# Kernel tuning notes

Hardware: AMD Instinct MI355X
Metric: run time of the kernel (lower is better)

Reference implementation:

```python
import jax, jax.numpy as jnp
import numpy as np

RATE = 2          # attention_rate from __init__
SOFTMAX_SCALE = 10.0  # standard contextual-attention temperature
EPS = 1e-8


def setup_inputs() -> dict:
    key = jax.random.key(0)
    k1, k2 = jax.random.split(key)
    x = jax.random.normal(k1, (1, 128, 192, 192), dtype=jnp.float32)
    # binary hole mask: 1 = hole (to be filled), 0 = valid background
    mask = (jax.random.uniform(k2, (1, 1, 192, 192)) < 0.25).astype(jnp.float32)
    return {"x": x, "mask": mask}


def reference(x, mask):
    b, c, h, w = x.shape
    r = RATE
    hs, ws = h // r, w // r
    n = hs * ws

    # F.interpolate(..., mode='nearest') downsample == strided slice when divisible
    xs = x[:, :, ::r, ::r]            # [b, c, hs, ws]
    ms = mask[:, :, ::r, ::r]         # [b, 1, hs, ws]

    feat = xs.reshape(b, c, n)        # queries (raw) and keys (normalized)
    keys = feat / (jnp.sqrt(jnp.sum(feat * feat, axis=1, keepdims=True)) + EPS)

    # conv-based correlation == all-pairs inner product with normalized bg patches
    scores = jnp.einsum('bcn,bcm->bnm', feat, keys) * SOFTMAX_SCALE  # [b, n, n]

    valid = (ms.reshape(b, 1, n) == 0.0)  # background key locations
    scores = jnp.where(valid, scores, -1e4)
    attn = jax.nn.softmax(scores, axis=-1)
    attn = attn * valid                   # zero out hole keys exactly

    # extract non-overlapping r x r patches from full-res x: [b, n, c*r*r]
    patches = (x.reshape(b, c, hs, r, ws, r)
                 .transpose(0, 2, 4, 1, 3, 5)
                 .reshape(b, n, c * r * r))

    # transposed-conv reconstruction == weighted sum of patches, folded back
    recon = jnp.einsum('bnm,bmd->bnd', attn, patches)   # [b, n, c*r*r]
    recon_img = (recon.reshape(b, hs, ws, c, r, r)
                      .transpose(0, 3, 1, 4, 2, 5)
                      .reshape(b, c, h, w))

    # composite: keep known pixels, fill holes with attended reconstruction
    return x * (1.0 - mask) + recon_img * mask
```

## Files before the change

### kernel.cpp

```cpp
#include <hip/hip_runtime.h>
#include <hip/hip_bf16.h>

typedef _Float16 f16x8 __attribute__((ext_vector_type(8)));
typedef _Float16 f16x4 __attribute__((ext_vector_type(4)));
typedef float    f32x4 __attribute__((ext_vector_type(4)));

#define HW   36864
#define W_   192
#define NS   9216
#define CCH  128
#define DV   512
#define ROWS 64
#define KV   64
#define NT   144

__global__ __launch_bounds__(256) void prep_vt_kernel(const float* __restrict__ x,
        _Float16* __restrict__ Vt, _Float16* __restrict__ F16)
{
    int m = blockIdx.x * 256 + threadIdx.x;
    int d = blockIdx.y;
    int c = d >> 2, di = (d >> 1) & 1, dj = d & 1;
    int i = m / 96, j = m - i * 96;
    float v = x[c * HW + (2 * i + di) * W_ + (2 * j + dj)];
    _Float16 h = (_Float16)v;
    Vt[(size_t)d * NS + m] = h;
    if ((d & 3) == 0) F16[m * CCH + c] = h;
}

__global__ __launch_bounds__(64) void prep_csv_kernel(const _Float16* __restrict__ F16,
        const float* __restrict__ mask, float* __restrict__ csv)
{
    int m = blockIdx.x;
    int t = threadIdx.x;
    float a = (float)F16[m * CCH + 2 * t];
    float b = (float)F16[m * CCH + 2 * t + 1];
    float ss = a * a + b * b;
    #pragma unroll
    for (int off = 1; off <= 32; off <<= 1)
        ss += __shfl_xor(ss, off);
    if (t == 0) {
        int i = m / 96, j = m - i * 96;
        float ms = mask[(2 * i) * W_ + 2 * j];
        csv[m] = (ms == 0.0f) ? 10.0f / (sqrtf(ss) + 1e-8f) : 0.0f;
    }
}

template<int KT>
__global__ __launch_bounds__(256, 3) void flash_kernel(const _Float16* __restrict__ F16,
        const _Float16* __restrict__ Vt, const float* __restrict__ csv,
        _Float16* __restrict__ po, float* __restrict__ av)
{
    constexpr int SPLT = NT / KT;
    __shared__ __align__(16) _Float16 Kb[2][KV * CCH];
    __shared__ __align__(16) _Float16 Pb[2][ROWS * KV];
    __shared__ __align__(16) float    abuf[2][ROWS];
    __shared__ __align__(16) int      flags[2][4];
    __shared__ __align__(16) float    lbuf[ROWS];

    const int tid  = threadIdx.x;
    const int wv   = tid >> 6;
    const int lane = tid & 63;
    const int g    = lane >> 4, c16 = lane & 15;
    const int flat = blockIdx.x;
    const int sp   = flat % SPLT;
    const int rest = flat / SPLT;
    const int n0   = (rest >> 1) * ROWS;
    const int d0   = (rest & 1) * 256;
    const int t0   = sp * KT;
    const int sw   = c16 & 7;

    auto stageK = [&](int nb, int t) {
        #pragma unroll
        for (int j = 0; j < 4; ++j) {
            const int key  = wv * 16 + j * 4 + g;
            const int csrc = (c16 & 8) | ((c16 & 7) ^ (key & 7));
            __builtin_amdgcn_global_load_lds(
                (const __attribute__((address_space(1))) void*)
                    (F16 + (size_t)(t * KV + key) * CCH + csrc * 8),
                (__attribute__((address_space(3))) void*)
                    (&Kb[nb][(wv * 16 + j * 4) * CCH]),
                16, 0, 0);
        }
    };

    f16x8 q[4];
    #pragma unroll
    for (int kk = 0; kk < 4; ++kk)
        q[kk] = *(const f16x8*)(F16 + (n0 + wv * 16 + c16) * CCH + kk * 32 + g * 8);

    f32x4 o[4][4];
    #pragma unroll
    for (int rf = 0; rf < 4; ++rf)
        #pragma unroll
        for (int df = 0; df < 4; ++df) o[rf][df] = 0.0f;
    float m_run = -1e30f, l_run = 0.0f;

    const _Float16* vbase = Vt + (size_t)(d0 + wv * 64 + c16) * NS + g * 8;

    stageK(0, t0);
    __syncthreads();

    for (int tl = 0; tl < KT; ++tl) {
        const int buf = tl & 1;
        const int m0  = (t0 + tl) * KV;

        f16x8 vreg[8];
        #pragma unroll
        for (int kf = 0; kf < 2; ++kf)
            #pragma unroll
            for (int df = 0; df < 4; ++df)
                vreg[kf * 4 + df] = *(const f16x8*)(vbase + (size_t)(df * 16) * NS
                                                    + m0 + kf * 32);

        f32x4 s[4];
        #pragma unroll
        for (int cf = 0; cf < 4; ++cf) s[cf] = 0.0f;
        #pragma unroll
        for (int cf = 0; cf < 4; ++cf) {
            const _Float16* kr = &Kb[buf][(cf * 16 + c16) * CCH];
            #pragma unroll
            for (int kk = 0; kk < 4; ++kk) {
                const int c  = kk * 4 + g;
                const int cc = (c & 8) | ((c & 7) ^ sw);
                s[cf] = __builtin_amdgcn_mfma_f32_16x16x32_f16(
                            *(const f16x8*)(kr + cc * 8), q[kk], s[cf], 0, 0, 0);
            }
        }

        f32x4 cs[4];
        #pragma unroll
        for (int cf = 0; cf < 4; ++cf)
            cs[cf] = *(const f32x4*)(csv + m0 + cf * 16 + g * 4);

        float tm = -1e30f;
        #pragma unroll
        for (int cf = 0; cf < 4; ++cf)
            #pragma unroll
            for (int r = 0; r < 4; ++r)
                tm = fmaxf(tm, (cs[cf][r] > 0.0f) ? s[cf][r] * cs[cf][r] : -1e30f);
        tm = fmaxf(tm, __shfl_xor(tm, 16));
        tm = fmaxf(tm, __shfl_xor(tm, 32));

        float al = 1.0f;
        const bool trig = __any(tm > m_run + 8.0f);
        if (trig) {
            float nm = fmaxf(m_run, tm);
            al = __expf(m_run - nm);
            l_run *= al; m_run = nm;
        }
        if (lane == 0) flags[buf][wv] = trig ? 1 : 0;
        if (g == 0)    abuf[buf][wv * 16 + c16] = al;

        float ps = 0.0f;
        const int prow = wv * 16 + c16;
        #pragma unroll
        for (int cf = 0; cf < 4; ++cf) {
            f16x4 ph;
            #pragma unroll
            for (int r = 0; r < 4; ++r) {
                float e = (cs[cf][r] > 0.0f) ? __expf(s[cf][r] * cs[cf][r] - m_run) : 0.0f;
                ps += e;
                ph[r] = (_Float16)e;
            }
            const int ch = (cf * 2 + (g >> 1)) ^ sw;
            *(f16x4*)(&Pb[buf][prow * KV + ch * 8 + (g & 1) * 4]) = ph;
        }
        ps += __shfl_xor(ps, 16);
        ps += __shfl_xor(ps, 32);
        l_run += ps;

        if (tl + 1 < KT) stageK(buf ^ 1, t0 + tl + 1);

        __syncthreads();

        {
            const int4 fl = *(const int4*)(&flags[buf][0]);
            if (fl.x | fl.y | fl.z | fl.w) {
                #pragma unroll
                for (int rf = 0; rf < 4; ++rf) {
                    f32x4 a4 = *(const f32x4*)(&abuf[buf][rf * 16 + g * 4]);
                    #pragma unroll
                    for (int df = 0; df < 4; ++df)
                        #pragma unroll
                        for (int r = 0; r < 4; ++r) o[rf][df][r] *= a4[r];
                }
            }
        }
        #pragma unroll
        for (int kf = 0; kf < 2; ++kf) {
            f16x8 pa[4];
            #pragma unroll
            for (int rf = 0; rf < 4; ++rf)
                pa[rf] = *(const f16x8*)(&Pb[buf][(rf * 16 + c16) * KV
                                                  + (((kf * 4 + g) ^ sw) * 8)]);
            #pragma unroll
            for (int df = 0; df < 4; ++df)
                #pragma unroll
                for (int rf = 0; rf < 4; ++rf)
                    o[rf][df] = __builtin_amdgcn_mfma_f32_16x16x32_f16(
                                    pa[rf], vreg[kf * 4 + df], o[rf][df], 0, 0, 0);
        }
    }

    if (g == 0) {
        lbuf[wv * 16 + c16] = (l_run > 0.0f) ? 1.0f / l_run : 0.0f;
        if (d0 == 0)
            av[sp * NS + n0 + wv * 16 + c16] =
                (l_run > 0.0f) ? m_run + __logf(l_run) : -1e30f;
    }
    __syncthreads();
    #pragma unroll
    for (int rf = 0; rf < 4; ++rf) {
        f32x4 li = *(const f32x4*)(&lbuf[rf * 16 + g * 4]);
        #pragma unroll
        for (int df = 0; df < 4; ++df) {
            f16x4 res;
            #pragma unroll
            for (int r = 0; r < 4; ++r) res[r] = (_Float16)(o[rf][df][r] * li[r]);
            *(f16x4*)(po + ((size_t)sp * DV + d0 + wv * 64 + df * 16 + c16) * NS
                          + n0 + rf * 16 + g * 4) = res;
        }
    }
}

template<int S>
__global__ __launch_bounds__(192) void combine_kernel(const float* __restrict__ x,
        const float* __restrict__ mask, const _Float16* __restrict__ po,
        const float* __restrict__ av, float* __restrict__ out)
{
    int i = blockIdx.x;
    int c = blockIdx.y;
    int w = threadIdx.x;
    int n = i * 96 + (w >> 1);

    float A = -1e30f;
    #pragma unroll
    for (int s = 0; s < S; ++s) A = fmaxf(A, av[s * NS + n]);
    float wt[S], wsum = 0.0f;
    #pragma unroll
    for (int s = 0; s < S; ++s) {
        float a = av[s * NS + n];
        float e = (a > -1e29f) ? __expf(a - A) : 0.0f;
        wt[s] = e; wsum += e;
    }
    float invw = (wsum > 0.0f) ? 1.0f / wsum : 0.0f;

    #pragma unroll
    for (int di = 0; di < 2; ++di) {
        int h = 2 * i + di;
        int d = c * 4 + di * 2 + (w & 1);
        float rv = 0.0f;
        #pragma unroll
        for (int s = 0; s < S; ++s)
            rv += wt[s] * (float)po[((size_t)s * DV + d) * NS + n];
        rv *= invw;
        float xv = x[c * HW + h * W_ + w];
        float mv = mask[h * W_ + w];
        out[c * HW + h * W_ + w] = xv * (1.0f - mv) + rv * mv;
    }
}

extern "C" void kernel_launch(void* const* d_in, const int* in_sizes, int n_in,
                              void* d_out, int out_size, void* d_ws, size_t ws_size,
                              hipStream_t stream) {
    const float* x    = (const float*)d_in[0];
    const float* mask = (const float*)d_in[1];
    float* out = (float*)d_out;

    char* ws = (char*)d_ws;
    _Float16* Vt  = (_Float16*)(ws);
    _Float16* F16 = (_Float16*)(ws + 9437184);
    float*    csv = (float*)   (ws + 11796480);
    float*    av  = (float*)   (ws + 11833344);
    _Float16* po  = (_Float16*)(ws + 12128256);

    prep_vt_kernel <<<dim3(36, 512), 256, 0, stream>>>(x, Vt, F16);
    prep_csv_kernel<<<NS, 64, 0, stream>>>(F16, mask, csv);

    const size_t base = 12128256ull;
    if (ws_size >= base + 8ull * 9437184ull) {
        flash_kernel<18><<<288 * 8, 256, 0, stream>>>(F16, Vt, csv, po, av);
        combine_kernel<8><<<dim3(96, 128), 192, 0, stream>>>(x, mask, po, av, out);
    } else {
        flash_kernel<36><<<288 * 4, 256, 0, stream>>>(F16, Vt, csv, po, av);
        combine_kernel<4><<<dim3(96, 128), 192, 0, stream>>>(x, mask, po, av, out);
    }
}
```

Measured before the change: 341.7 us.

## Use exp2 softmax with additive mask bias, earlier K prefetch, MFMA priority

Folds log2(e) into the per-key scale and adds a precomputed additive bias (-60000 for hole keys), so the inner loop becomes an FMA plus exp2 with no select. The K tile prefetch is issued at the top of each iteration so it overlaps the QK MFMAs. Global address offsets are precomputed, and s_setprio raises wave priority around the MFMA blocks. It adds a second small per-key array read each tile and changes the log-sum-exp output to base-2 scaling. The initial running max becomes a finite sentinel, which risks wrong handling when every key in a split is masked.

```diff
diff --git a/kernel.cpp b/kernel.cpp
--- a/kernel.cpp
+++ b/kernel.cpp
@@ -13,6 +13,11 @@
 #define ROWS 64
 #define KV   64
 #define NT   144
+#define LOG2E 1.44269504089f
+#define LN2   0.69314718056f
+#define THR2  11.5417f
+
+#define EXP2(x) __builtin_exp2f(x)
 
 __global__ __launch_bounds__(256) void prep_vt_kernel(const float* __restrict__ x,
         _Float16* __restrict__ Vt, _Float16* __restrict__ F16)
@@ -28,7 +33,7 @@
 }
 
 __global__ __launch_bounds__(64) void prep_csv_kernel(const _Float16* __restrict__ F16,
-        const float* __restrict__ mask, float* __restrict__ csv)
+        const float* __restrict__ mask, float* __restrict__ csv, float* __restrict__ csb)
 {
     int m = blockIdx.x;
     int t = threadIdx.x;
@@ -41,14 +46,16 @@
     if (t == 0) {
         int i = m / 96, j = m - i * 96;
         float ms = mask[(2 * i) * W_ + 2 * j];
-        csv[m] = (ms == 0.0f) ? 10.0f / (sqrtf(ss) + 1e-8f) : 0.0f;
+        bool valid = (ms == 0.0f);
+        csv[m] = valid ? 10.0f * LOG2E / (sqrtf(ss) + 1e-8f) : 0.0f;
+        csb[m] = valid ? 0.0f : -60000.0f;
     }
 }
 
 template<int KT>
 __global__ __launch_bounds__(256, 3) void flash_kernel(const _Float16* __restrict__ F16,
         const _Float16* __restrict__ Vt, const float* __restrict__ csv,
-        _Float16* __restrict__ po, float* __restrict__ av)
+        const float* __restrict__ csb, _Float16* __restrict__ po, float* __restrict__ av)
 {
     constexpr int SPLT = NT / KT;
     __shared__ __align__(16) _Float16 Kb[2][KV * CCH];
@@ -69,19 +76,30 @@
     const int t0   = sp * KT;
     const int sw   = c16 & 7;
 
+    int koff[4];
+    #pragma unroll
+    for (int j = 0; j < 4; ++j) {
+        const int key  = wv * 16 + j * 4 + g;
+        const int csrc = (c16 & 8) | ((c16 & 7) ^ (key & 7));
+        koff[j] = (key * CCH + csrc * 8) * 2;
+    }
     auto stageK = [&](int nb, int t) {
-        #pragma unroll
-        for (int j = 0; j < 4; ++j) {
-            const int key  = wv * 16 + j * 4 + g;
-            const int csrc = (c16 & 8) | ((c16 & 7) ^ (key & 7));
+        const char* src = (const char*)F16 + (size_t)t * (KV * CCH * 2);
+        #pragma unroll
+        for (int j = 0; j < 4; ++j)
             __builtin_amdgcn_global_load_lds(
-                (const __attribute__((address_space(1))) void*)
-                    (F16 + (size_t)(t * KV + key) * CCH + csrc * 8),
-                (__attribute__((address_space(3))) void*)
-                    (&Kb[nb][(wv * 16 + j * 4) * CCH]),
+                (const __attribute__((address_space(1))) void*)(src + koff[j]),
+                (__attribute__((address_space(3))) void*)(&Kb[nb][(wv * 16 + j * 4) * CCH]),
                 16, 0, 0);
-        }
     };
+
+    int voff[8];
+    #pragma unroll
+    for (int kf = 0; kf < 2; ++kf)
+        #pragma unroll
+        for (int df = 0; df < 4; ++df)
+            voff[kf * 4 + df] = (int)(((size_t)(d0 + wv * 64 + df * 16 + c16) * NS
+                                       + kf * 32 + g * 8) * 2);
 
     f16x8 q[4];
     #pragma unroll
@@ -93,9 +111,7 @@
     for (int rf = 0; rf < 4; ++rf)
         #pragma unroll
         for (int df = 0; df < 4; ++df) o[rf][df] = 0.0f;
-    float m_run = -1e30f, l_run = 0.0f;
-
-    const _Float16* vbase = Vt + (size_t)(d0 + wv * 64 + c16) * NS + g * 8;
+    float m_run = -20000.0f, l_run = 0.0f;
 
     stageK(0, t0);
     __syncthreads();
@@ -104,17 +120,18 @@
         const int buf = tl & 1;
         const int m0  = (t0 + tl) * KV;
 
+        if (tl + 1 < KT) stageK(buf ^ 1, t0 + tl + 1);
+
+        const char* vt = (const char*)Vt + (size_t)m0 * 2;
         f16x8 vreg[8];
         #pragma unroll
-        for (int kf = 0; kf < 2; ++kf)
-            #pragma unroll
-            for (int df = 0; df < 4; ++df)
-                vreg[kf * 4 + df] = *(const f16x8*)(vbase + (size_t)(df * 16) * NS
-                                                    + m0 + kf * 32);
+        for (int i = 0; i < 8; ++i)
+            vreg[i] = *(const f16x8*)(vt + voff[i]);
 
         f32x4 s[4];
         #pragma unroll
         for (int cf = 0; cf < 4; ++cf) s[cf] = 0.0f;
+        __builtin_amdgcn_s_setprio(1);
         #pragma unroll
         for (int cf = 0; cf < 4; ++cf) {
             const _Float16* kr = &Kb[buf][(cf * 16 + c16) * CCH];
@@ -126,26 +143,33 @@
                             *(const f16x8*)(kr + cc * 8), q[kk], s[cf], 0, 0, 0);
             }
         }
-
-        f32x4 cs[4];
+        __builtin_amdgcn_s_setprio(0);
+
+        const float* csvt = csv + m0;
+        const float* csbt = csb + m0;
+        f32x4 cs[4], cb[4];
+        #pragma unroll
+        for (int cf = 0; cf < 4; ++cf) {
+            cs[cf] = *(const f32x4*)(csvt + cf * 16 + g * 4);
+            cb[cf] = *(const f32x4*)(csbt + cf * 16 + g * 4);
+        }
+
+        float tm = -1e30f;
         #pragma unroll
         for (int cf = 0; cf < 4; ++cf)
-            cs[cf] = *(const f32x4*)(csv + m0 + cf * 16 + g * 4);
-
-        float tm = -1e30f;
-        #pragma unroll
-        for (int cf = 0; cf < 4; ++cf)
-            #pragma unroll
-            for (int r = 0; r < 4; ++r)
-                tm = fmaxf(tm, (cs[cf][r] > 0.0f) ? s[cf][r] * cs[cf][r] : -1e30f);
+            #pragma unroll
+            for (int r = 0; r < 4; ++r) {
+                s[cf][r] = __builtin_fmaf(s[cf][r], cs[cf][r], cb[cf][r]);
+                tm = fmaxf(tm, s[cf][r]);
+            }
         tm = fmaxf(tm, __shfl_xor(tm, 16));
         tm = fmaxf(tm, __shfl_xor(tm, 32));
 
         float al = 1.0f;
-        const bool trig = __any(tm > m_run + 8.0f);
+        const bool trig = __any(tm > m_run + THR2);
         if (trig) {
             float nm = fmaxf(m_run, tm);
-            al = __expf(m_run - nm);
+            al = EXP2(m_run - nm);
             l_run *= al; m_run = nm;
         }
         if (lane == 0) flags[buf][wv] = trig ? 1 : 0;
@@ -155,21 +179,18 @@
         const int prow = wv * 16 + c16;
         #pragma unroll
         for (int cf = 0; cf < 4; ++cf) {
-            f16x4 ph;
-            #pragma unroll
-            for (int r = 0; r < 4; ++r) {
-                float e = (cs[cf][r] > 0.0f) ? __expf(s[cf][r] * cs[cf][r] - m_run) : 0.0f;
-                ps += e;
-                ph[r] = (_Float16)e;
-            }
+            float e0 = EXP2(s[cf][0] - m_run);
+            float e1 = EXP2(s[cf][1] - m_run);
+            float e2 = EXP2(s[cf][2] - m_run);
+            float e3 = EXP2(s[cf][3] - m_run);
+            ps += (e0 + e1) + (e2 + e3);
+            f16x4 ph = { (_Float16)e0, (_Float16)e1, (_Float16)e2, (_Float16)e3 };
             const int ch = (cf * 2 + (g >> 1)) ^ sw;
             *(f16x4*)(&Pb[buf][prow * KV + ch * 8 + (g & 1) * 4]) = ph;
         }
         ps += __shfl_xor(ps, 16);
         ps += __shfl_xor(ps, 32);
         l_run += ps;
-
-        if (tl + 1 < KT) stageK(buf ^ 1, t0 + tl + 1);
 
         __syncthreads();
 
@@ -186,6 +207,7 @@
                 }
             }
         }
+        __builtin_amdgcn_s_setprio(1);
         #pragma unroll
         for (int kf = 0; kf < 2; ++kf) {
             f16x8 pa[4];
@@ -200,13 +222,14 @@
                     o[rf][df] = __builtin_amdgcn_mfma_f32_16x16x32_f16(
                                     pa[rf], vreg[kf * 4 + df], o[rf][df], 0, 0, 0);
         }
+        __builtin_amdgcn_s_setprio(0);
     }
 
     if (g == 0) {
         lbuf[wv * 16 + c16] = (l_run > 0.0f) ? 1.0f / l_run : 0.0f;
         if (d0 == 0)
             av[sp * NS + n0 + wv * 16 + c16] =
-                (l_run > 0.0f) ? m_run + __logf(l_run) : -1e30f;
+                (l_run > 0.0f) ? m_run * LN2 + __logf(l_run) : -1e30f;
     }
     __syncthreads();
     #pragma unroll
@@ -271,18 +294,19 @@
     _Float16* Vt  = (_Float16*)(ws);
     _Float16* F16 = (_Float16*)(ws + 9437184);
     float*    csv = (float*)   (ws + 11796480);
-    float*    av  = (float*)   (ws + 11833344);
-    _Float16* po  = (_Float16*)(ws + 12128256);
+    float*    csb = (float*)   (ws + 11833344);
+    float*    av  = (float*)   (ws + 11870208);
+    _Float16* po  = (_Float16*)(ws + 12165120);
 
     prep_vt_kernel <<<dim3(36, 512), 256, 0, stream>>>(x, Vt, F16);
-    prep_csv_kernel<<<NS, 64, 0, stream>>>(F16, mask, csv);
-
-    const size_t base = 12128256ull;
+    prep_csv_kernel<<<NS, 64, 0, stream>>>(F16, mask, csv, csb);
+
+    const size_t base = 12165120ull;
     if (ws_size >= base + 8ull * 9437184ull) {
-        flash_kernel<18><<<288 * 8, 256, 0, stream>>>(F16, Vt, csv, po, av);
+        flash_kernel<18><<<288 * 8, 256, 0, stream>>>(F16, Vt, csv, csb, po, av);
         combine_kernel<8><<<dim3(96, 128), 192, 0, stream>>>(x, mask, po, av, out);
     } else {
-        flash_kernel<36><<<288 * 4, 256, 0, stream>>>(F16, Vt, csv, po, av);
+        flash_kernel<36><<<288 * 4, 256, 0, stream>>>(F16, Vt, csv, csb, po, av);
         combine_kernel<4><<<dim3(96, 128), 192, 0, stream>>>(x, mask, po, av, out);
     }
 }
```

New measurement: 528.3 us. 1.55x slower.

## Halve key tile to 32, use exp2 with prescaled scores, raise occupancy, add setprio

Applied to the files above, without the earlier changes.

Cuts the flash kernel's key tile from 64 to 32 keys and doubles the tile count per split, so the K/P shared buffers and the score and V registers shrink. Launch bounds are raised to 4 waves per SIMD to fit more blocks per CU. The softmax moves to base-2 by folding log2(e) into the per-key scale, so exp2 is used directly, masking is applied once, and the rescale threshold and final logsumexp are adjusted to match. s_setprio is added around the MFMA sections, and the P swizzle changes to suit the narrower tile. Smaller tiles mean twice as many loop iterations and barriers per block, with less MFMA work to hide them.

```diff
diff --git a/kernel.cpp b/kernel.cpp
--- a/kernel.cpp
+++ b/kernel.cpp
@@ -11,8 +11,12 @@
 #define CCH  128
 #define DV   512
 #define ROWS 64
-#define KV   64
-#define NT   144
+#define KV   32
+#define NT2  288
+#define LOG2E 1.44269504089f
+#define LN2   0.69314718056f
+#define THR2  11.5417f
+#define EXP2(x) __builtin_exp2f(x)
 
 __global__ __launch_bounds__(256) void prep_vt_kernel(const float* __restrict__ x,
         _Float16* __restrict__ Vt, _Float16* __restrict__ F16)
@@ -41,16 +45,16 @@
     if (t == 0) {
         int i = m / 96, j = m - i * 96;
         float ms = mask[(2 * i) * W_ + 2 * j];
-        csv[m] = (ms == 0.0f) ? 10.0f / (sqrtf(ss) + 1e-8f) : 0.0f;
+        csv[m] = (ms == 0.0f) ? 10.0f * LOG2E / (sqrtf(ss) + 1e-8f) : 0.0f;
     }
 }
 
 template<int KT>
-__global__ __launch_bounds__(256, 3) void flash_kernel(const _Float16* __restrict__ F16,
+__global__ __launch_bounds__(256, 4) void flash_kernel(const _Float16* __restrict__ F16,
         const _Float16* __restrict__ Vt, const float* __restrict__ csv,
         _Float16* __restrict__ po, float* __restrict__ av)
 {
-    constexpr int SPLT = NT / KT;
+    constexpr int SPLT = NT2 / KT;
     __shared__ __align__(16) _Float16 Kb[2][KV * CCH];
     __shared__ __align__(16) _Float16 Pb[2][ROWS * KV];
     __shared__ __align__(16) float    abuf[2][ROWS];
@@ -71,14 +75,14 @@
 
     auto stageK = [&](int nb, int t) {
         #pragma unroll
-        for (int j = 0; j < 4; ++j) {
-            const int key  = wv * 16 + j * 4 + g;
+        for (int j = 0; j < 2; ++j) {
+            const int key  = wv * 8 + j * 4 + g;
             const int csrc = (c16 & 8) | ((c16 & 7) ^ (key & 7));
             __builtin_amdgcn_global_load_lds(
                 (const __attribute__((address_space(1))) void*)
                     (F16 + (size_t)(t * KV + key) * CCH + csrc * 8),
                 (__attribute__((address_space(3))) void*)
-                    (&Kb[nb][(wv * 16 + j * 4) * CCH]),
+                    (&Kb[nb][(wv * 8 + j * 4) * CCH]),
                 16, 0, 0);
         }
     };
@@ -93,7 +97,7 @@
     for (int rf = 0; rf < 4; ++rf)
         #pragma unroll
         for (int df = 0; df < 4; ++df) o[rf][df] = 0.0f;
-    float m_run = -1e30f, l_run = 0.0f;
+    float m_run = -20000.0f, l_run = 0.0f;
 
     const _Float16* vbase = Vt + (size_t)(d0 + wv * 64 + c16) * NS + g * 8;
 
@@ -104,19 +108,16 @@
         const int buf = tl & 1;
         const int m0  = (t0 + tl) * KV;
 
-        f16x8 vreg[8];
-        #pragma unroll
-        for (int kf = 0; kf < 2; ++kf)
-            #pragma unroll
-            for (int df = 0; df < 4; ++df)
-                vreg[kf * 4 + df] = *(const f16x8*)(vbase + (size_t)(df * 16) * NS
-                                                    + m0 + kf * 32);
-
-        f32x4 s[4];
-        #pragma unroll
-        for (int cf = 0; cf < 4; ++cf) s[cf] = 0.0f;
-        #pragma unroll
-        for (int cf = 0; cf < 4; ++cf) {
+        f16x8 vreg[4];
+        #pragma unroll
+        for (int df = 0; df < 4; ++df)
+            vreg[df] = *(const f16x8*)(vbase + (size_t)(df * 16) * NS + m0);
+
+        f32x4 s[2];
+        s[0] = 0.0f; s[1] = 0.0f;
+        __builtin_amdgcn_s_setprio(1);
+        #pragma unroll
+        for (int cf = 0; cf < 2; ++cf) {
             const _Float16* kr = &Kb[buf][(cf * 16 + c16) * CCH];
             #pragma unroll
             for (int kk = 0; kk < 4; ++kk) {
@@ -126,26 +127,29 @@
                             *(const f16x8*)(kr + cc * 8), q[kk], s[cf], 0, 0, 0);
             }
         }
-
-        f32x4 cs[4];
-        #pragma unroll
-        for (int cf = 0; cf < 4; ++cf)
-            cs[cf] = *(const f32x4*)(csv + m0 + cf * 16 + g * 4);
+        __builtin_amdgcn_s_setprio(0);
+
+        f32x4 cs[2];
+        cs[0] = *(const f32x4*)(csv + m0 + g * 4);
+        cs[1] = *(const f32x4*)(csv + m0 + 16 + g * 4);
 
         float tm = -1e30f;
         #pragma unroll
-        for (int cf = 0; cf < 4; ++cf)
-            #pragma unroll
-            for (int r = 0; r < 4; ++r)
-                tm = fmaxf(tm, (cs[cf][r] > 0.0f) ? s[cf][r] * cs[cf][r] : -1e30f);
+        for (int cf = 0; cf < 2; ++cf)
+            #pragma unroll
+            for (int r = 0; r < 4; ++r) {
+                float v = (cs[cf][r] > 0.0f) ? s[cf][r] * cs[cf][r] : -60000.0f;
+                s[cf][r] = v;
+                tm = fmaxf(tm, v);
+            }
         tm = fmaxf(tm, __shfl_xor(tm, 16));
         tm = fmaxf(tm, __shfl_xor(tm, 32));
 
         float al = 1.0f;
-        const bool trig = __any(tm > m_run + 8.0f);
+        const bool trig = __any(tm > m_run + THR2);
         if (trig) {
             float nm = fmaxf(m_run, tm);
-            al = __expf(m_run - nm);
+            al = EXP2(m_run - nm);
             l_run *= al; m_run = nm;
         }
         if (lane == 0) flags[buf][wv] = trig ? 1 : 0;
@@ -154,15 +158,14 @@
         float ps = 0.0f;
         const int prow = wv * 16 + c16;
         #pragma unroll
-        for (int cf = 0; cf < 4; ++cf) {
-            f16x4 ph;
-            #pragma unroll
-            for (int r = 0; r < 4; ++r) {
-                float e = (cs[cf][r] > 0.0f) ? __expf(s[cf][r] * cs[cf][r] - m_run) : 0.0f;
-                ps += e;
-                ph[r] = (_Float16)e;
-            }
-            const int ch = (cf * 2 + (g >> 1)) ^ sw;
+        for (int cf = 0; cf < 2; ++cf) {
+            float e0 = EXP2(s[cf][0] - m_run);
+            float e1 = EXP2(s[cf][1] - m_run);
+            float e2 = EXP2(s[cf][2] - m_run);
+            float e3 = EXP2(s[cf][3] - m_run);
+            ps += (e0 + e1) + (e2 + e3);
+            f16x4 ph = { (_Float16)e0, (_Float16)e1, (_Float16)e2, (_Float16)e3 };
+            const int ch = (cf * 2 + (g >> 1)) ^ (c16 & 3);
             *(f16x4*)(&Pb[buf][prow * KV + ch * 8 + (g & 1) * 4]) = ph;
         }
         ps += __shfl_xor(ps, 16);
@@ -186,27 +189,28 @@
                 }
             }
         }
-        #pragma unroll
-        for (int kf = 0; kf < 2; ++kf) {
+        __builtin_amdgcn_s_setprio(1);
+        {
             f16x8 pa[4];
             #pragma unroll
             for (int rf = 0; rf < 4; ++rf)
                 pa[rf] = *(const f16x8*)(&Pb[buf][(rf * 16 + c16) * KV
-                                                  + (((kf * 4 + g) ^ sw) * 8)]);
+                                                  + ((g ^ (c16 & 3)) * 8)]);
             #pragma unroll
             for (int df = 0; df < 4; ++df)
                 #pragma unroll
                 for (int rf = 0; rf < 4; ++rf)
                     o[rf][df] = __builtin_amdgcn_mfma_f32_16x16x32_f16(
-                                    pa[rf], vreg[kf * 4 + df], o[rf][df], 0, 0, 0);
-        }
+                                    pa[rf], vreg[df], o[rf][df], 0, 0, 0);
+        }
+        __builtin_amdgcn_s_setprio(0);
     }
 
     if (g == 0) {
         lbuf[wv * 16 + c16] = (l_run > 0.0f) ? 1.0f / l_run : 0.0f;
         if (d0 == 0)
             av[sp * NS + n0 + wv * 16 + c16] =
-                (l_run > 0.0f) ? m_run + __logf(l_run) : -1e30f;
+                (l_run > 0.0f) ? m_run * LN2 + __logf(l_run) : -1e30f;
     }
     __syncthreads();
     #pragma unroll
@@ -279,10 +283,10 @@
 
     const size_t base = 12128256ull;
     if (ws_size >= base + 8ull * 9437184ull) {
-        flash_kernel<18><<<288 * 8, 256, 0, stream>>>(F16, Vt, csv, po, av);
+        flash_kernel<36><<<288 * 8, 256, 0, stream>>>(F16, Vt, csv, po, av);
         combine_kernel<8><<<dim3(96, 128), 192, 0, stream>>>(x, mask, po, av, out);
     } else {
-        flash_kernel<36><<<288 * 4, 256, 0, stream>>>(F16, Vt, csv, po, av);
+        flash_kernel<72><<<288 * 4, 256, 0, stream>>>(F16, Vt, csv, po, av);
         combine_kernel<4><<<dim3(96, 128), 192, 0, stream>>>(x, mask, po, av, out);
     }
 }
```

Measured after the change: 462.9 us. 1.35x slower.

## Software-pipeline QK and PV MFMAs across tiles with base-2 softmax

Applied to the files above, without the earlier changes.

Restructures the flash-attention loop so the PV matmul for the previous tile is interleaved with the QK matmul of the current tile. This lets the matrix units overlap with the softmax of the next step, and V loads are issued after the MFMAs to hide their latency. The softmax moves to exp2 by folding log2(e) into the key scale, and masked keys now go through a large negative constant instead of a branch. s_setprio hints are added around the MFMA blocks. In exchange there are more live registers (vreg carried across iterations) and occupancy may suffer.

```diff
diff --git a/kernel.cpp b/kernel.cpp
--- a/kernel.cpp
+++ b/kernel.cpp
@@ -13,6 +13,10 @@
 #define ROWS 64
 #define KV   64
 #define NT   144
+#define LOG2E 1.44269504089f
+#define LN2   0.69314718056f
+#define THR2  11.5417f
+#define EXP2(x) __builtin_exp2f(x)
 
 __global__ __launch_bounds__(256) void prep_vt_kernel(const float* __restrict__ x,
         _Float16* __restrict__ Vt, _Float16* __restrict__ F16)
@@ -41,7 +45,7 @@
     if (t == 0) {
         int i = m / 96, j = m - i * 96;
         float ms = mask[(2 * i) * W_ + 2 * j];
-        csv[m] = (ms == 0.0f) ? 10.0f / (sqrtf(ss) + 1e-8f) : 0.0f;
+        csv[m] = (ms == 0.0f) ? 10.0f * LOG2E / (sqrtf(ss) + 1e-8f) : 0.0f;
     }
 }
 
@@ -93,31 +97,83 @@
     for (int rf = 0; rf < 4; ++rf)
         #pragma unroll
         for (int df = 0; df < 4; ++df) o[rf][df] = 0.0f;
-    float m_run = -1e30f, l_run = 0.0f;
+    float m_run = -20000.0f, l_run = 0.0f;
 
     const _Float16* vbase = Vt + (size_t)(d0 + wv * 64 + c16) * NS + g * 8;
+    f16x8 vreg[8];
 
     stageK(0, t0);
     __syncthreads();
 
-    for (int tl = 0; tl < KT; ++tl) {
-        const int buf = tl & 1;
-        const int m0  = (t0 + tl) * KV;
-
-        f16x8 vreg[8];
-        #pragma unroll
-        for (int kf = 0; kf < 2; ++kf)
-            #pragma unroll
-            for (int df = 0; df < 4; ++df)
-                vreg[kf * 4 + df] = *(const f16x8*)(vbase + (size_t)(df * 16) * NS
-                                                    + m0 + kf * 32);
-
+    auto softmax_store = [&](int kb, int m0, f32x4* s) {
+        f32x4 cs[4];
+        #pragma unroll
+        for (int cf = 0; cf < 4; ++cf)
+            cs[cf] = *(const f32x4*)(csv + m0 + cf * 16 + g * 4);
+        float tm = -1e30f;
+        #pragma unroll
+        for (int cf = 0; cf < 4; ++cf)
+            #pragma unroll
+            for (int r = 0; r < 4; ++r) {
+                float v = (cs[cf][r] > 0.0f) ? s[cf][r] * cs[cf][r] : -60000.0f;
+                s[cf][r] = v;
+                tm = fmaxf(tm, v);
+            }
+        tm = fmaxf(tm, __shfl_xor(tm, 16));
+        tm = fmaxf(tm, __shfl_xor(tm, 32));
+        float al = 1.0f;
+        const bool trig = __any(tm > m_run + THR2);
+        if (trig) {
+            float nm = fmaxf(m_run, tm);
+            al = EXP2(m_run - nm);
+            l_run *= al; m_run = nm;
+        }
+        if (lane == 0) flags[kb][wv] = trig ? 1 : 0;
+        if (g == 0)    abuf[kb][wv * 16 + c16] = al;
+        float ps = 0.0f;
+        const int prow = wv * 16 + c16;
+        #pragma unroll
+        for (int cf = 0; cf < 4; ++cf) {
+            float e0 = EXP2(s[cf][0] - m_run);
+            float e1 = EXP2(s[cf][1] - m_run);
+            float e2 = EXP2(s[cf][2] - m_run);
+            float e3 = EXP2(s[cf][3] - m_run);
+            ps += (e0 + e1) + (e2 + e3);
+            f16x4 ph = { (_Float16)e0, (_Float16)e1, (_Float16)e2, (_Float16)e3 };
+            const int ch = (cf * 2 + (g >> 1)) ^ sw;
+            *(f16x4*)(&Pb[kb][prow * KV + ch * 8 + (g & 1) * 4]) = ph;
+        }
+        ps += __shfl_xor(ps, 16);
+        ps += __shfl_xor(ps, 32);
+        l_run += ps;
+    };
+
+    auto rescale = [&](int pb) {
+        const int4 fl = *(const int4*)(&flags[pb][0]);
+        if (fl.x | fl.y | fl.z | fl.w) {
+            #pragma unroll
+            for (int rf = 0; rf < 4; ++rf) {
+                f32x4 a4 = *(const f32x4*)(&abuf[pb][rf * 16 + g * 4]);
+                #pragma unroll
+                for (int df = 0; df < 4; ++df)
+                    #pragma unroll
+                    for (int r = 0; r < 4; ++r) o[rf][df][r] *= a4[r];
+            }
+        }
+    };
+
+    {
+        const int m0 = t0 * KV;
+        #pragma unroll
+        for (int i = 0; i < 8; ++i)
+            vreg[i] = *(const f16x8*)(vbase + (size_t)((i & 3) * 16) * NS + m0 + (i >> 2) * 32);
         f32x4 s[4];
         #pragma unroll
         for (int cf = 0; cf < 4; ++cf) s[cf] = 0.0f;
+        __builtin_amdgcn_s_setprio(1);
         #pragma unroll
         for (int cf = 0; cf < 4; ++cf) {
-            const _Float16* kr = &Kb[buf][(cf * 16 + c16) * CCH];
+            const _Float16* kr = &Kb[0][(cf * 16 + c16) * CCH];
             #pragma unroll
             for (int kk = 0; kk < 4; ++kk) {
                 const int c  = kk * 4 + g;
@@ -126,72 +182,93 @@
                             *(const f16x8*)(kr + cc * 8), q[kk], s[cf], 0, 0, 0);
             }
         }
-
-        f32x4 cs[4];
-        #pragma unroll
-        for (int cf = 0; cf < 4; ++cf)
-            cs[cf] = *(const f32x4*)(csv + m0 + cf * 16 + g * 4);
-
-        float tm = -1e30f;
-        #pragma unroll
-        for (int cf = 0; cf < 4; ++cf)
-            #pragma unroll
-            for (int r = 0; r < 4; ++r)
-                tm = fmaxf(tm, (cs[cf][r] > 0.0f) ? s[cf][r] * cs[cf][r] : -1e30f);
-        tm = fmaxf(tm, __shfl_xor(tm, 16));
-        tm = fmaxf(tm, __shfl_xor(tm, 32));
-
-        float al = 1.0f;
-        const bool trig = __any(tm > m_run + 8.0f);
-        if (trig) {
-            float nm = fmaxf(m_run, tm);
-            al = __expf(m_run - nm);
-            l_run *= al; m_run = nm;
-        }
-        if (lane == 0) flags[buf][wv] = trig ? 1 : 0;
-        if (g == 0)    abuf[buf][wv * 16 + c16] = al;
-
-        float ps = 0.0f;
-        const int prow = wv * 16 + c16;
-        #pragma unroll
-        for (int cf = 0; cf < 4; ++cf) {
-            f16x4 ph;
-            #pragma unroll
-            for (int r = 0; r < 4; ++r) {
-                float e = (cs[cf][r] > 0.0f) ? __expf(s[cf][r] * cs[cf][r] - m_run) : 0.0f;
-                ps += e;
-                ph[r] = (_Float16)e;
-            }
-            const int ch = (cf * 2 + (g >> 1)) ^ sw;
-            *(f16x4*)(&Pb[buf][prow * KV + ch * 8 + (g & 1) * 4]) = ph;
-        }
-        ps += __shfl_xor(ps, 16);
-        ps += __shfl_xor(ps, 32);
-        l_run += ps;
-
-        if (tl + 1 < KT) stageK(buf ^ 1, t0 + tl + 1);
-
+        __builtin_amdgcn_s_setprio(0);
+        softmax_store(0, m0, s);
+        if (KT > 1) stageK(1, t0 + 1);
         __syncthreads();
-
+    }
+
+    for (int tl = 1; tl < KT; ++tl) {
+        const int pb = (tl - 1) & 1;
+        const int kb = tl & 1;
+        const int m0 = (t0 + tl) * KV;
+
+        rescale(pb);
+
+        f32x4 s[4];
+        #pragma unroll
+        for (int cf = 0; cf < 4; ++cf) s[cf] = 0.0f;
+
+        __builtin_amdgcn_s_setprio(1);
         {
-            const int4 fl = *(const int4*)(&flags[buf][0]);
-            if (fl.x | fl.y | fl.z | fl.w) {
-                #pragma unroll
-                for (int rf = 0; rf < 4; ++rf) {
-                    f32x4 a4 = *(const f32x4*)(&abuf[buf][rf * 16 + g * 4]);
-                    #pragma unroll
-                    for (int df = 0; df < 4; ++df)
-                        #pragma unroll
-                        for (int r = 0; r < 4; ++r) o[rf][df][r] *= a4[r];
+            f16x8 pa[4];
+            #pragma unroll
+            for (int rf = 0; rf < 4; ++rf)
+                pa[rf] = *(const f16x8*)(&Pb[pb][(rf * 16 + c16) * KV + ((g ^ sw) * 8)]);
+            #pragma unroll
+            for (int cf = 0; cf < 2; ++cf) {
+                const _Float16* kr = &Kb[kb][(cf * 16 + c16) * CCH];
+                #pragma unroll
+                for (int kk = 0; kk < 4; ++kk) {
+                    const int c  = kk * 4 + g;
+                    const int cc = (c & 8) | ((c & 7) ^ sw);
+                    s[cf] = __builtin_amdgcn_mfma_f32_16x16x32_f16(
+                                *(const f16x8*)(kr + cc * 8), q[kk], s[cf], 0, 0, 0);
                 }
             }
-        }
+            #pragma unroll
+            for (int df = 0; df < 4; ++df)
+                #pragma unroll
+                for (int rf = 0; rf < 4; ++rf)
+                    o[rf][df] = __builtin_amdgcn_mfma_f32_16x16x32_f16(
+                                    pa[rf], vreg[df], o[rf][df], 0, 0, 0);
+        }
+        {
+            f16x8 pa[4];
+            #pragma unroll
+            for (int rf = 0; rf < 4; ++rf)
+                pa[rf] = *(const f16x8*)(&Pb[pb][(rf * 16 + c16) * KV + (((4 + g) ^ sw) * 8)]);
+            #pragma unroll
+            for (int cf = 2; cf < 4; ++cf) {
+                const _Float16* kr = &Kb[kb][(cf * 16 + c16) * CCH];
+                #pragma unroll
+                for (int kk = 0; kk < 4; ++kk) {
+                    const int c  = kk * 4 + g;
+                    const int cc = (c & 8) | ((c & 7) ^ sw);
+                    s[cf] = __builtin_amdgcn_mfma_f32_16x16x32_f16(
+                                *(const f16x8*)(kr + cc * 8), q[kk], s[cf], 0, 0, 0);
+                }
+            }
+            #pragma unroll
+            for (int df = 0; df < 4; ++df)
+                #pragma unroll
+                for (int rf = 0; rf < 4; ++rf)
+                    o[rf][df] = __builtin_amdgcn_mfma_f32_16x16x32_f16(
+                                    pa[rf], vreg[4 + df], o[rf][df], 0, 0, 0);
+        }
+        __builtin_amdgcn_s_setprio(0);
+
+        #pragma unroll
+        for (int i = 0; i < 8; ++i)
+            vreg[i] = *(const f16x8*)(vbase + (size_t)((i & 3) * 16) * NS + m0 + (i >> 2) * 32);
+
+        softmax_store(kb, m0, s);
+
+        if (tl + 1 < KT) stageK((tl + 1) & 1, t0 + tl + 1);
+
+        __syncthreads();
+    }
+
+    {
+        const int pb = (KT - 1) & 1;
+        rescale(pb);
+        __builtin_amdgcn_s_setprio(1);
         #pragma unroll
         for (int kf = 0; kf < 2; ++kf) {
             f16x8 pa[4];
             #pragma unroll
             for (int rf = 0; rf < 4; ++rf)
-                pa[rf] = *(const f16x8*)(&Pb[buf][(rf * 16 + c16) * KV
+                pa[rf] = *(const f16x8*)(&Pb[pb][(rf * 16 + c16) * KV
                                                   + (((kf * 4 + g) ^ sw) * 8)]);
             #pragma unroll
             for (int df = 0; df < 4; ++df)
@@ -200,13 +277,14 @@
                     o[rf][df] = __builtin_amdgcn_mfma_f32_16x16x32_f16(
                                     pa[rf], vreg[kf * 4 + df], o[rf][df], 0, 0, 0);
         }
+        __builtin_amdgcn_s_setprio(0);
     }
 
     if (g == 0) {
         lbuf[wv * 16 + c16] = (l_run > 0.0f) ? 1.0f / l_run : 0.0f;
         if (d0 == 0)
             av[sp * NS + n0 + wv * 16 + c16] =
-                (l_run > 0.0f) ? m_run + __logf(l_run) : -1e30f;
+                (l_run > 0.0f) ? m_run * LN2 + __logf(l_run) : -1e30f;
     }
     __syncthreads();
     #pragma unroll
```

Result: slower. 379.0 us (+10.9%).
